# Kernel tuning notes

Hardware: AMD Instinct MI355X
Metric: run time of the kernel (lower is better)

The kernel has to match this reference:

```python
import jax, jax.numpy as jnp
import numpy as np

NUM_NODES = 10000  # fixed by input spec: edge_index values in [0, 10000)


def setup_inputs() -> dict:
    key = jax.random.key(0)
    k1, k2, k3 = jax.random.split(key, 3)
    N, E, D_IN, D_OUT = NUM_NODES, 320000, 256, 256
    x = jax.random.normal(k1, (N, D_IN), dtype=jnp.float32)
    edge_index = jax.random.randint(k2, (2, E), 0, N, dtype=jnp.int64)
    # ensure node N-1 appears so num_nodes == N as in the torch code
    edge_index = edge_index.at[0, 0].set(N - 1)
    # xavier_uniform for [D_IN, D_OUT]
    limit = float(np.sqrt(6.0 / (D_IN + D_OUT)))
    weight = jax.random.uniform(k3, (D_IN, D_OUT), dtype=jnp.float32,
                                minval=-limit, maxval=limit)
    return {"x": x, "edge_index": edge_index, "weight": weight}


def _normalize_adjacency(edge_index, num_nodes):
    src, dst = edge_index[0], edge_index[1]
    ones = jnp.ones(src.shape[0], dtype=jnp.float32)
    # symmetric binarized adjacency: adj[i,j] = adj[j,i] = 1 (set, not add)
    adj = jnp.zeros((num_nodes, num_nodes), dtype=jnp.float32)
    adj = adj.at[src, dst].max(ones)
    adj = adj.at[dst, src].max(ones)
    # one round of self-loops: adj += I
    adj = adj + jnp.eye(num_nodes, dtype=jnp.float32)
    deg = jnp.sum(adj, axis=1)                    # [N]
    dinv = 1.0 / jnp.sqrt(deg)                    # [N]
    # D^-1/2 A D^-1/2 via broadcasting (equivalent to diag mms)
    return adj * dinv[:, None] * dinv[None, :]


def reference(x, edge_index, weight):
    adj = _normalize_adjacency(edge_index, NUM_NODES)  # [N, N]
    h = adj @ x                                        # [N, D_IN]
    return h @ weight                                  # [N, D_OUT]
```

## Files before the change

kernel.cpp:

```cpp
#include <hip/hip_runtime.h>
#include <hip/hip_bf16.h>
#include <stdint.h>

#define N_NODES   10000
#define D_FEAT    256
#define E_EDGES   320000
#define ROW_WORDS 313
#define LIST_CAP  1024

#define NB     1000
#define RPB    10
#define B_CAP  1024
#define NBLK_E 313
#define NBLK_W 64
#define NBLK_C 1000
#define NBLK_G 625
#define COLSTR 128

#define LDSTR 264

typedef __attribute__((ext_vector_type(4))) float float4v;
typedef _Float16 half8  __attribute__((ext_vector_type(8)));
typedef _Float16 half4v __attribute__((ext_vector_type(4)));

__device__ __forceinline__ float h2f_lo(uint32_t u) {
    union { uint32_t u; _Float16 h[2]; } v; v.u = u; return (float)v.h[0];
}
__device__ __forceinline__ float h2f_hi(uint32_t u) {
    union { uint32_t u; _Float16 h[2]; } v; v.u = u; return (float)v.h[1];
}


__global__ void __launch_bounds__(1024)
scatter_wcast(const int* __restrict__ ei, uint32_t* __restrict__ bitmap,
              const float* __restrict__ w, _Float16* __restrict__ wt) {
    __shared__ float st[1024];
    int t = threadIdx.x;

    if (blockIdx.x >= NBLK_E) {
        int kb = (blockIdx.x - NBLK_E) * 4;
        int k = kb + (t >> 8), n = t & 255;
        st[(n << 2) | (t >> 8)] = w[(size_t)k * D_FEAT + n];
        __syncthreads();
        if (t < 256) {
            half4v o = { (_Float16)st[t * 4 + 0], (_Float16)st[t * 4 + 1],
                         (_Float16)st[t * 4 + 2], (_Float16)st[t * 4 + 3] };
            *(half4v*)&wt[(size_t)t * D_FEAT + kb] = o;
        }
        return;
    }

    int e = blockIdx.x * 1024 + t;
    if (e >= E_EDGES) return;
    int s = ei[e], d = ei[E_EDGES + e];
    if ((uint32_t)s >= N_NODES || (uint32_t)d >= N_NODES) return;
    atomicOr(&bitmap[(size_t)s * ROW_WORDS + (d >> 5)], 1u << (d & 31));
    atomicOr(&bitmap[(size_t)d * ROW_WORDS + (s >> 5)], 1u << (s & 31));
}

__global__ void __launch_bounds__(1024)
gemm_popc(const uint32_t* __restrict__ bitmap, float* __restrict__ dinv,
          const float* __restrict__ x, const _Float16* __restrict__ wt,
          _Float16* __restrict__ yw) {
    __shared__ __align__(16) _Float16 a_lds[16 * LDSTR];
    int t = threadIdx.x;

    if (blockIdx.x < NBLK_G) {
        int r0 = blockIdx.x * 16;
        int row = t >> 6, c4 = (t & 63) * 4;
        float4v xv = *(const float4v*)(x + (size_t)(r0 + row) * D_FEAT + c4);
        half4v h = { (_Float16)xv[0], (_Float16)xv[1],
                     (_Float16)xv[2], (_Float16)xv[3] };
        *(half4v*)&a_lds[row * LDSTR + c4] = h;
        __syncthreads();
        int wv = t >> 6, lane = t & 63;
        int quad = lane >> 4, r = lane & 15;
        int ct = wv;
        const _Float16* pb = wt + (size_t)(ct * 16 + r) * D_FEAT + quad * 8;
        float4v acc = {0.f, 0.f, 0.f, 0.f};
        #pragma unroll
        for (int kk = 0; kk < D_FEAT; kk += 32) {
            half8 a = *(const half8*)&a_lds[r * LDSTR + kk + quad * 8];
            half8 b = *(const half8*)(pb + kk);
            acc = __builtin_amdgcn_mfma_f32_16x16x32_f16(a, b, acc, 0, 0, 0);
        }
        int colg = ct * 16 + r;
        #pragma unroll
        for (int u = 0; u < 4; u++)
            yw[(size_t)(r0 + quad * 4 + u) * D_FEAT + colg] = (_Float16)acc[u];
        return;
    }

    int wv = t >> 6, lane = t & 63;
    int i = (blockIdx.x - NBLK_G) * 16 + wv;
    const uint32_t* rb = bitmap + (size_t)i * ROW_WORDS;
    int pop = 0;
    #pragma unroll
    for (int k = 0; k < 5; k++) {
        int w = lane + 64 * k;
        if (w < ROW_WORDS) pop += __popc(rb[w]);
    }
    #pragma unroll
    for (int off = 32; off > 0; off >>= 1) pop += __shfl_xor(pop, off, 64);
    if (lane == 0) dinv[i] = 1.0f / sqrtf((float)(pop + 1));
}

__global__ void __launch_bounds__(256)
spmm_bm(const uint32_t* __restrict__ bitmap, const float* __restrict__ dinv,
        const _Float16* __restrict__ ywp, float* __restrict__ out) {
    __shared__ __align__(16) uint32_t lists[4][LIST_CAP];
    const uint16_t* yw = (const uint16_t*)ywp;
    int wv = threadIdx.x >> 6, lane = threadIdx.x & 63;
    int i = blockIdx.x * 4 + wv;
    uint32_t* list = lists[wv];
    const uint32_t* rb = bitmap + (size_t)i * ROW_WORDS;

    uint32_t wbits[5]; int tot = 0;
    #pragma unroll
    for (int k = 0; k < 5; k++) {
        int w = lane + 64 * k;
        uint32_t b = (w < ROW_WORDS) ? rb[w] : 0u;
        wbits[k] = b;
        tot += __popc(b);
    }
    int incl = tot;
    #pragma unroll
    for (int off = 1; off < 64; off <<= 1) {
        int v = __shfl_up(incl, off, 64);
        if (lane >= off) incl += v;
    }
    uint32_t p = (uint32_t)(incl - tot);
    uint32_t deg = (uint32_t)__shfl(incl, 63, 64);
    #pragma unroll
    for (int k = 0; k < 5; k++) {
        uint32_t bits = wbits[k];
        uint32_t cbase = (uint32_t)(lane + 64 * k) << 5;
        while (bits) {
            if (p < LIST_CAP) list[p] = cbase + (uint32_t)__builtin_ctz(bits);
            p++;
            bits &= bits - 1;
        }
    }
    if (deg > LIST_CAP) deg = LIST_CAP;

    float di = dinv[i];
    size_t ch = (size_t)lane * 4;
    float4v z = {0.f, 0.f, 0.f, 0.f};
    float4v a0 = z, a1 = z, a2 = z, a3 = z, a4 = z, a5 = z, a6 = z, a7 = z;
    uint32_t t8 = deg & ~7u;
    uint32_t t = 0;
    for (; t < t8; t += 8) {
        uint4 jv0 = *(const uint4*)&list[t];
        uint4 jv1 = *(const uint4*)&list[t + 4];
        uint32_t j0 = jv0.x, j1 = jv0.y, j2 = jv0.z, j3 = jv0.w;
        uint32_t j4 = jv1.x, j5 = jv1.y, j6 = jv1.z, j7 = jv1.w;
        float d0 = dinv[j0], d1 = dinv[j1], d2 = dinv[j2], d3 = dinv[j3];
        float d4 = dinv[j4], d5 = dinv[j5], d6 = dinv[j6], d7 = dinv[j7];
        uint2 g0 = *(const uint2*)(yw + (size_t)j0 * D_FEAT + ch);
        uint2 g1 = *(const uint2*)(yw + (size_t)j1 * D_FEAT + ch);
        uint2 g2 = *(const uint2*)(yw + (size_t)j2 * D_FEAT + ch);
        uint2 g3 = *(const uint2*)(yw + (size_t)j3 * D_FEAT + ch);
        uint2 g4 = *(const uint2*)(yw + (size_t)j4 * D_FEAT + ch);
        uint2 g5 = *(const uint2*)(yw + (size_t)j5 * D_FEAT + ch);
        uint2 g6 = *(const uint2*)(yw + (size_t)j6 * D_FEAT + ch);
        uint2 g7 = *(const uint2*)(yw + (size_t)j7 * D_FEAT + ch);
        a0[0] += d0 * h2f_lo(g0.x); a0[1] += d0 * h2f_hi(g0.x);
        a0[2] += d0 * h2f_lo(g0.y); a0[3] += d0 * h2f_hi(g0.y);
        a1[0] += d1 * h2f_lo(g1.x); a1[1] += d1 * h2f_hi(g1.x);
        a1[2] += d1 * h2f_lo(g1.y); a1[3] += d1 * h2f_hi(g1.y);
        a2[0] += d2 * h2f_lo(g2.x); a2[1] += d2 * h2f_hi(g2.x);
        a2[2] += d2 * h2f_lo(g2.y); a2[3] += d2 * h2f_hi(g2.y);
        a3[0] += d3 * h2f_lo(g3.x); a3[1] += d3 * h2f_hi(g3.x);
        a3[2] += d3 * h2f_lo(g3.y); a3[3] += d3 * h2f_hi(g3.y);
        a4[0] += d4 * h2f_lo(g4.x); a4[1] += d4 * h2f_hi(g4.x);
        a4[2] += d4 * h2f_lo(g4.y); a4[3] += d4 * h2f_hi(g4.y);
        a5[0] += d5 * h2f_lo(g5.x); a5[1] += d5 * h2f_hi(g5.x);
        a5[2] += d5 * h2f_lo(g5.y); a5[3] += d5 * h2f_hi(g5.y);
        a6[0] += d6 * h2f_lo(g6.x); a6[1] += d6 * h2f_hi(g6.x);
        a6[2] += d6 * h2f_lo(g6.y); a6[3] += d6 * h2f_hi(g6.y);
        a7[0] += d7 * h2f_lo(g7.x); a7[1] += d7 * h2f_hi(g7.x);
        a7[2] += d7 * h2f_lo(g7.y); a7[3] += d7 * h2f_hi(g7.y);
    }
    for (; t < deg; t++) {
        uint32_t j = list[t];
        float dj = dinv[j];
        uint2 g = *(const uint2*)(yw + (size_t)j * D_FEAT + ch);
        a0[0] += dj * h2f_lo(g.x); a0[1] += dj * h2f_hi(g.x);
        a0[2] += dj * h2f_lo(g.y); a0[3] += dj * h2f_hi(g.y);
    }
    uint2 gs = *(const uint2*)(yw + (size_t)i * D_FEAT + ch);
    a1[0] += di * h2f_lo(gs.x); a1[1] += di * h2f_hi(gs.x);
    a1[2] += di * h2f_lo(gs.y); a1[3] += di * h2f_hi(gs.y);
    float4v acc = ((a0 + a1) + (a2 + a3)) + ((a4 + a5) + (a6 + a7));
    *(float4v*)(out + (size_t)i * D_FEAT + ch) = di * acc;
}


__global__ void __launch_bounds__(1024)
fill_sort(const int* __restrict__ ei, uint32_t* __restrict__ bucketbuf,
          uint32_t* __restrict__ cursors,
          const float* __restrict__ w, _Float16* __restrict__ wt) {
    __shared__ uint32_t hist[1024];
    __shared__ uint32_t lofs[1024];
    __shared__ uint32_t base_s[1024];
    __shared__ uint32_t wsum[16];
    __shared__ uint32_t stage[2048];
    __shared__ uint16_t sbkt[2048];
    int t = threadIdx.x;

    if (blockIdx.x >= NBLK_E) {
        int kb = (blockIdx.x - NBLK_E) * 4;
        int k = kb + (t >> 8), n = t & 255;
        float* st = (float*)stage;
        st[(n << 2) | (t >> 8)] = w[(size_t)k * D_FEAT + n];
        __syncthreads();
        if (t < 256) {
            half4v o = { (_Float16)st[t * 4 + 0], (_Float16)st[t * 4 + 1],
                         (_Float16)st[t * 4 + 2], (_Float16)st[t * 4 + 3] };
            *(half4v*)&wt[(size_t)t * D_FEAT + kb] = o;
        }
        return;
    }

    int wv = t >> 6, lane = t & 63;
    hist[t] = 0;
    __syncthreads();
    int e = blockIdx.x * 1024 + t;
    int b0 = -1, b1 = -1; uint32_t ent0 = 0, ent1 = 0, s0 = 0, s1 = 0;
    if (e < E_EDGES) {
        int s = ei[e], d = ei[E_EDGES + e];
        if ((uint32_t)s < N_NODES && (uint32_t)d < N_NODES) {
            b0 = s / RPB; ent0 = ((uint32_t)(s - b0 * RPB) << 14) | (uint32_t)d;
            b1 = d / RPB; ent1 = ((uint32_t)(d - b1 * RPB) << 14) | (uint32_t)s;
            s0 = atomicAdd(&hist[b0], 1u);
            s1 = atomicAdd(&hist[b1], 1u);
        }
    }
    __syncthreads();
    uint32_t h = hist[t];
    uint32_t incl = h;
    #pragma unroll
    for (int off = 1; off < 64; off <<= 1) {
        uint32_t v = __shfl_up(incl, off, 64);
        if (lane >= off) incl += v;
    }
    if (lane == 63) wsum[wv] = incl;
    __syncthreads();
    if (wv == 0) {
        uint32_t s = (lane < 16) ? wsum[lane] : 0u;
        #pragma unroll
        for (int off = 1; off < 16; off <<= 1) {
            uint32_t v = __shfl_up(s, off, 64);
            if (lane >= off) s += v;
        }
        if (lane < 16) wsum[lane] = s;
    }
    __syncthreads();
    uint32_t wbase = wv ? wsum[wv - 1] : 0u;
    lofs[t] = incl + wbase;
    base_s[t] = h ? atomicAdd(&cursors[t], h) : 0u;
    __syncthreads();
    if (b0 >= 0) {
        uint32_t p0 = lofs[b0] - hist[b0] + s0;
        stage[p0] = ent0; sbkt[p0] = (uint16_t)b0;
        uint32_t p1 = lofs[b1] - hist[b1] + s1;
        stage[p1] = ent1; sbkt[p1] = (uint16_t)b1;
    }
    __syncthreads();
    uint32_t total = lofs[1023];
    for (uint32_t idx = t; idx < total; idx += 1024) {
        uint32_t b = sbkt[idx];
        uint32_t pos = base_s[b] + (idx - (lofs[b] - hist[b]));
        if (pos < B_CAP) bucketbuf[(size_t)b * B_CAP + pos] = stage[idx];
    }
}

__global__ void __launch_bounds__(1024)
csr_gemm(const uint32_t* __restrict__ bucketbuf, const uint32_t* __restrict__ cursors,
         uint32_t* __restrict__ row_deg, float* __restrict__ dinv,
         uint16_t* __restrict__ col,
         const float* __restrict__ x, const _Float16* __restrict__ wt,
         _Float16* __restrict__ yw) {
    __shared__ __align__(16) uint32_t smem[RPB * ROW_WORDS];
    int t = threadIdx.x;

    if (blockIdx.x >= NBLK_C) {
        _Float16* a_lds = (_Float16*)smem;
        int r0 = (blockIdx.x - NBLK_C) * 16;
        int row = t >> 6, c4 = (t & 63) * 4;
        float4v xv = *(const float4v*)(x + (size_t)(r0 + row) * D_FEAT + c4);
        half4v h = { (_Float16)xv[0], (_Float16)xv[1],
                     (_Float16)xv[2], (_Float16)xv[3] };
        *(half4v*)&a_lds[row * LDSTR + c4] = h;
        __syncthreads();
        int wv = t >> 6, lane = t & 63;
        int quad = lane >> 4, r = lane & 15;
        int ct = wv;
        const _Float16* pb = wt + (size_t)(ct * 16 + r) * D_FEAT + quad * 8;
        float4v acc = {0.f, 0.f, 0.f, 0.f};
        #pragma unroll
        for (int kk = 0; kk < D_FEAT; kk += 32) {
            half8 a = *(const half8*)&a_lds[r * LDSTR + kk + quad * 8];
            half8 b = *(const half8*)(pb + kk);
            acc = __builtin_amdgcn_mfma_f32_16x16x32_f16(a, b, acc, 0, 0, 0);
        }
        int colg = ct * 16 + r;
        #pragma unroll
        for (int u = 0; u < 4; u++)
            yw[(size_t)(r0 + quad * 4 + u) * D_FEAT + colg] = (_Float16)acc[u];
        return;
    }

    uint32_t* bm = smem;
    int b = blockIdx.x;
    for (int i = t; i < RPB * ROW_WORDS; i += 1024) bm[i] = 0;
    __syncthreads();
    uint32_t cnt = min(cursors[b], (uint32_t)B_CAP);
    const uint32_t* bb = bucketbuf + (size_t)b * B_CAP;
    for (uint32_t i = t; i < cnt; i += 1024) {
        uint32_t ent = bb[i];
        uint32_t lr = ent >> 14, d = ent & 0x3FFFu;
        atomicOr(&bm[lr * ROW_WORDS + (d >> 5)], 1u << (d & 31));
    }
    __syncthreads();
    int wv = t >> 6, lane = t & 63;
    if (wv < RPB) {
        int r = wv;
        int gi = b * RPB + r;
        uint32_t wb[5]; int tot = 0;
        #pragma unroll
        for (int k = 0; k < 5; k++) {
            int w = lane + 64 * k;
            uint32_t v = (w < ROW_WORDS) ? bm[r * ROW_WORDS + w] : 0u;
            wb[k] = v; tot += __popc(v);
        }
        int incl = tot;
        #pragma unroll
        for (int off = 1; off < 64; off <<= 1) {
            int v = __shfl_up(incl, off, 64);
            if (lane >= off) incl += v;
        }
        uint32_t total = (uint32_t)__shfl(incl, 63, 64);
        if (lane == 0) {
            row_deg[gi] = min(total, (uint32_t)COLSTR);
            dinv[gi]    = 1.0f / sqrtf((float)(total + 1u));
        }
        uint32_t p = (uint32_t)(incl - tot);
        #pragma unroll
        for (int k = 0; k < 5; k++) {
            uint32_t bits = wb[k];
            uint32_t cbase = (uint32_t)(lane + 64 * k) << 5;
            while (bits) {
                if (p < COLSTR)
                    col[(size_t)gi * COLSTR + p] =
                        (uint16_t)(cbase + (uint32_t)__builtin_ctz(bits));
                p++;
                bits &= bits - 1;
            }
        }
    }
}

__global__ void __launch_bounds__(256)
spmm_out(const uint32_t* __restrict__ row_deg, const float* __restrict__ dinv,
         const uint16_t* __restrict__ col, const _Float16* __restrict__ ywp,
         float* __restrict__ out) {
    const uint16_t* yw = (const uint16_t*)ywp;
    int wv = threadIdx.x >> 6, lane = threadIdx.x & 63;
    int half = lane >> 5, sl = lane & 31;
    int i = blockIdx.x * 4 + wv;
    uint32_t base = (uint32_t)i * COLSTR;
    uint32_t deg = min(row_deg[i], (uint32_t)COLSTR);
    float di = dinv[i];
    size_t ch = (size_t)sl * 8;
    float4v z = {0.f, 0.f, 0.f, 0.f};
    float4v accl[8], acch[8];
    #pragma unroll
    for (int k = 0; k < 8; k++) { accl[k] = z; acch[k] = z; }

    uint32_t hb = (uint32_t)(half << 3);
    uint4 cv = {0u, 0u, 0u, 0u};
    if (deg) cv = *(const uint4*)&col[base + hb];

    for (uint32_t t = 0; t < deg; t += 16) {
        uint4 cvn = {0u, 0u, 0u, 0u};
        uint32_t tn = t + 16;
        if (tn < deg) cvn = *(const uint4*)&col[base + tn + hb];
        uint32_t tb = t + hb;
        uint32_t jr[8];
        jr[0] = cv.x & 0xffffu; jr[1] = cv.x >> 16;
        jr[2] = cv.y & 0xffffu; jr[3] = cv.y >> 16;
        jr[4] = cv.z & 0xffffu; jr[5] = cv.z >> 16;
        jr[6] = cv.w & 0xffffu; jr[7] = cv.w >> 16;
        uint4 g[8]; float dk[8];
        #pragma unroll
        for (int k = 0; k < 8; k++) {
            uint32_t j = min(jr[k], (uint32_t)(N_NODES - 1));
            g[k]  = *(const uint4*)(yw + ((size_t)j << 8) + ch);
            dk[k] = dinv[j];
        }
        #pragma unroll
        for (int k = 0; k < 8; k++) {
            float d = (tb + (uint32_t)k < deg) ? dk[k] : 0.f;
            accl[k][0] += d * h2f_lo(g[k].x); accl[k][1] += d * h2f_hi(g[k].x);
            accl[k][2] += d * h2f_lo(g[k].y); accl[k][3] += d * h2f_hi(g[k].y);
            acch[k][0] += d * h2f_lo(g[k].z); acch[k][1] += d * h2f_hi(g[k].z);
            acch[k][2] += d * h2f_lo(g[k].w); acch[k][3] += d * h2f_hi(g[k].w);
        }
        cv = cvn;
    }

    if (half == 0) {
        const uint4 gs = *(const uint4*)(yw + ((size_t)i << 8) + ch);
        accl[0][0] += di * h2f_lo(gs.x); accl[0][1] += di * h2f_hi(gs.x);
        accl[0][2] += di * h2f_lo(gs.y); accl[0][3] += di * h2f_hi(gs.y);
        acch[0][0] += di * h2f_lo(gs.z); acch[0][1] += di * h2f_hi(gs.z);
        acch[0][2] += di * h2f_lo(gs.w); acch[0][3] += di * h2f_hi(gs.w);
    }

    float4v lo = ((accl[0] + accl[1]) + (accl[2] + accl[3])) +
                 ((accl[4] + accl[5]) + (accl[6] + accl[7]));
    float4v hi = ((acch[0] + acch[1]) + (acch[2] + acch[3])) +
                 ((acch[4] + acch[5]) + (acch[6] + acch[7]));
    #pragma unroll
    for (int u = 0; u < 4; u++) {
        lo[u] += __shfl_xor(lo[u], 32, 64);
        hi[u] += __shfl_xor(hi[u], 32, 64);
    }
    float4v res;
    if (half) res = hi; else res = lo;
    float* op = out + (size_t)i * D_FEAT + (size_t)sl * 8 + (half ? 4 : 0);
    *(float4v*)op = di * res;
}

extern "C" void kernel_launch(void* const* d_in, const int* in_sizes, int n_in,
                              void* d_out, int out_size, void* d_ws, size_t ws_size,
                              hipStream_t stream) {
    const float* x  = (const float*)d_in[0];
    const int*   ei = (const int*)d_in[1];
    const float* w  = (const float*)d_in[2];
    float* out = (float*)d_out;
    uint8_t* ws = (uint8_t*)d_ws;

    const size_t T1_DI   = 12520000;
    const size_t T1_WT   = 12560000;
    const size_t T1_YW   = 12691072;
    const size_t NEED_T1 = 17811072;

    const size_t BB_OFF   = 4096;
    const size_t RD_OFF   = 4100096;
    const size_t DI_OFF   = 4140096;
    const size_t WT_OFF   = 4180096;
    const size_t YW_OFF   = 4311168;
    const size_t COL_OFF  = 9431168;
    const size_t NEED_T2  = 11991168;

    if (ws_size >= NEED_T1) {
        uint32_t* bitmap = (uint32_t*)ws;
        float*    dinv   = (float*)(ws + T1_DI);
        _Float16* wt     = (_Float16*)(ws + T1_WT);
        _Float16* yw     = (_Float16*)(ws + T1_YW);

        hipMemsetAsync(bitmap, 0, 12520000, stream);
        scatter_wcast<<<NBLK_E + NBLK_W, 1024, 0, stream>>>(ei, bitmap, w, wt);
        gemm_popc    <<<NBLK_G + 625, 1024, 0, stream>>>(bitmap, dinv, x, wt, yw);
        spmm_bm      <<<N_NODES / 4, 256, 0, stream>>>(bitmap, dinv, yw, out);
    } else if (ws_size >= NEED_T2) {
        uint32_t* cursors   = (uint32_t*)ws;
        uint32_t* bucketbuf = (uint32_t*)(ws + BB_OFF);
        uint32_t* row_deg   = (uint32_t*)(ws + RD_OFF);
        float*    dinv      = (float*)(ws + DI_OFF);
        _Float16* wt        = (_Float16*)(ws + WT_OFF);
        _Float16* yw        = (_Float16*)(ws + YW_OFF);
        uint16_t* col       = (uint16_t*)(ws + COL_OFF);

        hipMemsetAsync(cursors, 0, 4096, stream);
        fill_sort<<<NBLK_E + NBLK_W, 1024, 0, stream>>>(ei, bucketbuf, cursors, w, wt);
        csr_gemm <<<NBLK_C + NBLK_G, 1024, 0, stream>>>(bucketbuf, cursors,
                                                        row_deg, dinv, col, x, wt, yw);
        spmm_out <<<N_NODES / 4, 256, 0, stream>>>(row_deg, dinv, col, yw, out);
    }
}
```

Baseline: 140.4 us.

## Fuse scatter, GEMM and SpMM into one cooperative persistent kernel with grid syncs

Replaces the three launches (scatter+weight cast, gemm+degree, bitmap SpMM) with a single cooperative kernel of 1024 blocks of 256 threads, using grid.sync between phases and grid-stride loops. The aim is to remove per-launch overhead and inter-kernel gaps. In exchange, blocks shrink from 1024 to 256 threads, each GEMM block now covers four column tiles per wave, and grid-wide barriers add their own latency. If the cooperative launch fails, it falls back to the CSR path.

Result: slower. 405.4 us (+188.7%).

```diff
diff --git a/kernel.cpp b/kernel.cpp
--- a/kernel.cpp
+++ b/kernel.cpp
@@ -1,6 +1,9 @@
 #include <hip/hip_runtime.h>
+#include <hip/hip_cooperative_groups.h>
 #include <hip/hip_bf16.h>
 #include <stdint.h>
+
+namespace cg = cooperative_groups;
 
 #define N_NODES   10000
 #define D_FEAT    256
@@ -18,6 +21,7 @@
 #define COLSTR 128
 
 #define LDSTR 264
+#define GRID_C 1024
 
 typedef __attribute__((ext_vector_type(4))) float float4v;
 typedef _Float16 half8  __attribute__((ext_vector_type(8)));
@@ -30,169 +34,162 @@
     union { uint32_t u; _Float16 h[2]; } v; v.u = u; return (float)v.h[1];
 }
 
-
-__global__ void __launch_bounds__(1024)
-scatter_wcast(const int* __restrict__ ei, uint32_t* __restrict__ bitmap,
-              const float* __restrict__ w, _Float16* __restrict__ wt) {
-    __shared__ float st[1024];
+__global__ void __launch_bounds__(256, 4)
+fused_gcn(const int* __restrict__ ei, uint32_t* __restrict__ bitmap,
+          const float* __restrict__ w, _Float16* __restrict__ wt,
+          const float* __restrict__ x, float* __restrict__ dinv,
+          _Float16* __restrict__ yw, float* __restrict__ out) {
+    cg::grid_group grid = cg::this_grid();
+    __shared__ __align__(16) uint8_t smem[16384];
     int t = threadIdx.x;
-
-    if (blockIdx.x >= NBLK_E) {
-        int kb = (blockIdx.x - NBLK_E) * 4;
-        int k = kb + (t >> 8), n = t & 255;
-        st[(n << 2) | (t >> 8)] = w[(size_t)k * D_FEAT + n];
+    int bid = blockIdx.x;
+    int wv = t >> 6, lane = t & 63;
+
+    if (bid < 64) {
+        float* st = (float*)smem;
+        int kb = bid * 4;
+        for (int idx = t; idx < 1024; idx += 256)
+            st[idx] = w[(size_t)kb * D_FEAT + idx];
         __syncthreads();
-        if (t < 256) {
-            half4v o = { (_Float16)st[t * 4 + 0], (_Float16)st[t * 4 + 1],
-                         (_Float16)st[t * 4 + 2], (_Float16)st[t * 4 + 3] };
-            *(half4v*)&wt[(size_t)t * D_FEAT + kb] = o;
-        }
-        return;
-    }
-
-    int e = blockIdx.x * 1024 + t;
-    if (e >= E_EDGES) return;
-    int s = ei[e], d = ei[E_EDGES + e];
-    if ((uint32_t)s >= N_NODES || (uint32_t)d >= N_NODES) return;
-    atomicOr(&bitmap[(size_t)s * ROW_WORDS + (d >> 5)], 1u << (d & 31));
-    atomicOr(&bitmap[(size_t)d * ROW_WORDS + (s >> 5)], 1u << (s & 31));
-}
-
-__global__ void __launch_bounds__(1024)
-gemm_popc(const uint32_t* __restrict__ bitmap, float* __restrict__ dinv,
-          const float* __restrict__ x, const _Float16* __restrict__ wt,
-          _Float16* __restrict__ yw) {
-    __shared__ __align__(16) _Float16 a_lds[16 * LDSTR];
-    int t = threadIdx.x;
-
-    if (blockIdx.x < NBLK_G) {
-        int r0 = blockIdx.x * 16;
-        int row = t >> 6, c4 = (t & 63) * 4;
-        float4v xv = *(const float4v*)(x + (size_t)(r0 + row) * D_FEAT + c4);
-        half4v h = { (_Float16)xv[0], (_Float16)xv[1],
-                     (_Float16)xv[2], (_Float16)xv[3] };
-        *(half4v*)&a_lds[row * LDSTR + c4] = h;
+        int n = t;
+        half4v o = { (_Float16)st[0 * 256 + n], (_Float16)st[1 * 256 + n],
+                     (_Float16)st[2 * 256 + n], (_Float16)st[3 * 256 + n] };
+        *(half4v*)&wt[(size_t)n * D_FEAT + kb] = o;
+    }
+    for (int e = bid * 256 + t; e < E_EDGES; e += GRID_C * 256) {
+        int s = ei[e], d = ei[E_EDGES + e];
+        if ((uint32_t)s < N_NODES && (uint32_t)d < N_NODES) {
+            atomicOr(&bitmap[(size_t)s * ROW_WORDS + (d >> 5)], 1u << (d & 31));
+            atomicOr(&bitmap[(size_t)d * ROW_WORDS + (s >> 5)], 1u << (s & 31));
+        }
+    }
+    grid.sync();
+
+    if (bid < NBLK_G) {
+        _Float16* a_lds = (_Float16*)smem;
+        int r0 = bid * 16;
+        for (int idx = t; idx < 1024; idx += 256) {
+            int row = idx >> 6, c4 = (idx & 63) * 4;
+            float4v xv = *(const float4v*)(x + (size_t)(r0 + row) * D_FEAT + c4);
+            half4v h = { (_Float16)xv[0], (_Float16)xv[1],
+                         (_Float16)xv[2], (_Float16)xv[3] };
+            *(half4v*)&a_lds[row * LDSTR + c4] = h;
+        }
         __syncthreads();
-        int wv = t >> 6, lane = t & 63;
         int quad = lane >> 4, r = lane & 15;
-        int ct = wv;
-        const _Float16* pb = wt + (size_t)(ct * 16 + r) * D_FEAT + quad * 8;
-        float4v acc = {0.f, 0.f, 0.f, 0.f};
-        #pragma unroll
-        for (int kk = 0; kk < D_FEAT; kk += 32) {
-            half8 a = *(const half8*)&a_lds[r * LDSTR + kk + quad * 8];
-            half8 b = *(const half8*)(pb + kk);
-            acc = __builtin_amdgcn_mfma_f32_16x16x32_f16(a, b, acc, 0, 0, 0);
-        }
-        int colg = ct * 16 + r;
-        #pragma unroll
-        for (int u = 0; u < 4; u++)
-            yw[(size_t)(r0 + quad * 4 + u) * D_FEAT + colg] = (_Float16)acc[u];
-        return;
-    }
-
-    int wv = t >> 6, lane = t & 63;
-    int i = (blockIdx.x - NBLK_G) * 16 + wv;
-    const uint32_t* rb = bitmap + (size_t)i * ROW_WORDS;
-    int pop = 0;
-    #pragma unroll
-    for (int k = 0; k < 5; k++) {
-        int w = lane + 64 * k;
-        if (w < ROW_WORDS) pop += __popc(rb[w]);
-    }
-    #pragma unroll
-    for (int off = 32; off > 0; off >>= 1) pop += __shfl_xor(pop, off, 64);
-    if (lane == 0) dinv[i] = 1.0f / sqrtf((float)(pop + 1));
-}
-
-__global__ void __launch_bounds__(256)
-spmm_bm(const uint32_t* __restrict__ bitmap, const float* __restrict__ dinv,
-        const _Float16* __restrict__ ywp, float* __restrict__ out) {
-    __shared__ __align__(16) uint32_t lists[4][LIST_CAP];
-    const uint16_t* yw = (const uint16_t*)ywp;
-    int wv = threadIdx.x >> 6, lane = threadIdx.x & 63;
-    int i = blockIdx.x * 4 + wv;
-    uint32_t* list = lists[wv];
-    const uint32_t* rb = bitmap + (size_t)i * ROW_WORDS;
-
-    uint32_t wbits[5]; int tot = 0;
-    #pragma unroll
-    for (int k = 0; k < 5; k++) {
-        int w = lane + 64 * k;
-        uint32_t b = (w < ROW_WORDS) ? rb[w] : 0u;
-        wbits[k] = b;
-        tot += __popc(b);
-    }
-    int incl = tot;
-    #pragma unroll
-    for (int off = 1; off < 64; off <<= 1) {
-        int v = __shfl_up(incl, off, 64);
-        if (lane >= off) incl += v;
-    }
-    uint32_t p = (uint32_t)(incl - tot);
-    uint32_t deg = (uint32_t)__shfl(incl, 63, 64);
-    #pragma unroll
-    for (int k = 0; k < 5; k++) {
-        uint32_t bits = wbits[k];
-        uint32_t cbase = (uint32_t)(lane + 64 * k) << 5;
-        while (bits) {
-            if (p < LIST_CAP) list[p] = cbase + (uint32_t)__builtin_ctz(bits);
-            p++;
-            bits &= bits - 1;
-        }
-    }
-    if (deg > LIST_CAP) deg = LIST_CAP;
-
-    float di = dinv[i];
-    size_t ch = (size_t)lane * 4;
-    float4v z = {0.f, 0.f, 0.f, 0.f};
-    float4v a0 = z, a1 = z, a2 = z, a3 = z, a4 = z, a5 = z, a6 = z, a7 = z;
-    uint32_t t8 = deg & ~7u;
-    uint32_t t = 0;
-    for (; t < t8; t += 8) {
-        uint4 jv0 = *(const uint4*)&list[t];
-        uint4 jv1 = *(const uint4*)&list[t + 4];
-        uint32_t j0 = jv0.x, j1 = jv0.y, j2 = jv0.z, j3 = jv0.w;
-        uint32_t j4 = jv1.x, j5 = jv1.y, j6 = jv1.z, j7 = jv1.w;
-        float d0 = dinv[j0], d1 = dinv[j1], d2 = dinv[j2], d3 = dinv[j3];
-        float d4 = dinv[j4], d5 = dinv[j5], d6 = dinv[j6], d7 = dinv[j7];
-        uint2 g0 = *(const uint2*)(yw + (size_t)j0 * D_FEAT + ch);
-        uint2 g1 = *(const uint2*)(yw + (size_t)j1 * D_FEAT + ch);
-        uint2 g2 = *(const uint2*)(yw + (size_t)j2 * D_FEAT + ch);
-        uint2 g3 = *(const uint2*)(yw + (size_t)j3 * D_FEAT + ch);
-        uint2 g4 = *(const uint2*)(yw + (size_t)j4 * D_FEAT + ch);
-        uint2 g5 = *(const uint2*)(yw + (size_t)j5 * D_FEAT + ch);
-        uint2 g6 = *(const uint2*)(yw + (size_t)j6 * D_FEAT + ch);
-        uint2 g7 = *(const uint2*)(yw + (size_t)j7 * D_FEAT + ch);
-        a0[0] += d0 * h2f_lo(g0.x); a0[1] += d0 * h2f_hi(g0.x);
-        a0[2] += d0 * h2f_lo(g0.y); a0[3] += d0 * h2f_hi(g0.y);
-        a1[0] += d1 * h2f_lo(g1.x); a1[1] += d1 * h2f_hi(g1.x);
-        a1[2] += d1 * h2f_lo(g1.y); a1[3] += d1 * h2f_hi(g1.y);
-        a2[0] += d2 * h2f_lo(g2.x); a2[1] += d2 * h2f_hi(g2.x);
-        a2[2] += d2 * h2f_lo(g2.y); a2[3] += d2 * h2f_hi(g2.y);
-        a3[0] += d3 * h2f_lo(g3.x); a3[1] += d3 * h2f_hi(g3.x);
-        a3[2] += d3 * h2f_lo(g3.y); a3[3] += d3 * h2f_hi(g3.y);
-        a4[0] += d4 * h2f_lo(g4.x); a4[1] += d4 * h2f_hi(g4.x);
-        a4[2] += d4 * h2f_lo(g4.y); a4[3] += d4 * h2f_hi(g4.y);
-        a5[0] += d5 * h2f_lo(g5.x); a5[1] += d5 * h2f_hi(g5.x);
-        a5[2] += d5 * h2f_lo(g5.y); a5[3] += d5 * h2f_hi(g5.y);
-        a6[0] += d6 * h2f_lo(g6.x); a6[1] += d6 * h2f_hi(g6.x);
-        a6[2] += d6 * h2f_lo(g6.y); a6[3] += d6 * h2f_hi(g6.y);
-        a7[0] += d7 * h2f_lo(g7.x); a7[1] += d7 * h2f_hi(g7.x);
-        a7[2] += d7 * h2f_lo(g7.y); a7[3] += d7 * h2f_hi(g7.y);
-    }
-    for (; t < deg; t++) {
-        uint32_t j = list[t];
-        float dj = dinv[j];
-        uint2 g = *(const uint2*)(yw + (size_t)j * D_FEAT + ch);
-        a0[0] += dj * h2f_lo(g.x); a0[1] += dj * h2f_hi(g.x);
-        a0[2] += dj * h2f_lo(g.y); a0[3] += dj * h2f_hi(g.y);
-    }
-    uint2 gs = *(const uint2*)(yw + (size_t)i * D_FEAT + ch);
-    a1[0] += di * h2f_lo(gs.x); a1[1] += di * h2f_hi(gs.x);
-    a1[2] += di * h2f_lo(gs.y); a1[3] += di * h2f_hi(gs.y);
-    float4v acc = ((a0 + a1) + (a2 + a3)) + ((a4 + a5) + (a6 + a7));
-    *(float4v*)(out + (size_t)i * D_FEAT + ch) = di * acc;
+        for (int s = 0; s < 4; s++) {
+            int ct = wv * 4 + s;
+            const _Float16* pb = wt + (size_t)(ct * 16 + r) * D_FEAT + quad * 8;
+            float4v acc = {0.f, 0.f, 0.f, 0.f};
+            #pragma unroll
+            for (int kk = 0; kk < D_FEAT; kk += 32) {
+                half8 a = *(const half8*)&a_lds[r * LDSTR + kk + quad * 8];
+                half8 b = *(const half8*)(pb + kk);
+                acc = __builtin_amdgcn_mfma_f32_16x16x32_f16(a, b, acc, 0, 0, 0);
+            }
+            int colg = ct * 16 + r;
+            #pragma unroll
+            for (int u = 0; u < 4; u++)
+                yw[(size_t)(r0 + quad * 4 + u) * D_FEAT + colg] = (_Float16)acc[u];
+        }
+    }
+    for (int i = bid * 4 + wv; i < N_NODES; i += GRID_C * 4) {
+        const uint32_t* rb = bitmap + (size_t)i * ROW_WORDS;
+        int pop = 0;
+        #pragma unroll
+        for (int k = 0; k < 5; k++) {
+            int ww = lane + 64 * k;
+            if (ww < ROW_WORDS) pop += __popc(rb[ww]);
+        }
+        #pragma unroll
+        for (int off = 32; off > 0; off >>= 1) pop += __shfl_xor(pop, off, 64);
+        if (lane == 0) dinv[i] = 1.0f / sqrtf((float)(pop + 1));
+    }
+    grid.sync();
+
+    const uint16_t* ywu = (const uint16_t*)yw;
+    uint32_t* list = (uint32_t*)smem + (size_t)wv * LIST_CAP;
+    for (int i = bid * 4 + wv; i < N_NODES; i += GRID_C * 4) {
+        const uint32_t* rb = bitmap + (size_t)i * ROW_WORDS;
+        uint32_t wbits[5]; int tot = 0;
+        #pragma unroll
+        for (int k = 0; k < 5; k++) {
+            int ww = lane + 64 * k;
+            uint32_t b = (ww < ROW_WORDS) ? rb[ww] : 0u;
+            wbits[k] = b;
+            tot += __popc(b);
+        }
+        int incl = tot;
+        #pragma unroll
+        for (int off = 1; off < 64; off <<= 1) {
+            int v = __shfl_up(incl, off, 64);
+            if (lane >= off) incl += v;
+        }
+        uint32_t p = (uint32_t)(incl - tot);
+        uint32_t deg = (uint32_t)__shfl(incl, 63, 64);
+        #pragma unroll
+        for (int k = 0; k < 5; k++) {
+            uint32_t bits = wbits[k];
+            uint32_t cbase = (uint32_t)(lane + 64 * k) << 5;
+            while (bits) {
+                if (p < LIST_CAP) list[p] = cbase + (uint32_t)__builtin_ctz(bits);
+                p++;
+                bits &= bits - 1;
+            }
+        }
+        if (deg > LIST_CAP) deg = LIST_CAP;
+
+        float di = dinv[i];
+        size_t ch = (size_t)lane * 4;
+        float4v z = {0.f, 0.f, 0.f, 0.f};
+        float4v a0 = z, a1 = z, a2 = z, a3 = z, a4 = z, a5 = z, a6 = z, a7 = z;
+        uint32_t t8 = deg & ~7u;
+        uint32_t tt = 0;
+        for (; tt < t8; tt += 8) {
+            uint4 jv0 = *(const uint4*)&list[tt];
+            uint4 jv1 = *(const uint4*)&list[tt + 4];
+            uint32_t j0 = jv0.x, j1 = jv0.y, j2 = jv0.z, j3 = jv0.w;
+            uint32_t j4 = jv1.x, j5 = jv1.y, j6 = jv1.z, j7 = jv1.w;
+            float d0 = dinv[j0], d1 = dinv[j1], d2 = dinv[j2], d3 = dinv[j3];
+            float d4 = dinv[j4], d5 = dinv[j5], d6 = dinv[j6], d7 = dinv[j7];
+            uint2 g0 = *(const uint2*)(ywu + (size_t)j0 * D_FEAT + ch);
+            uint2 g1 = *(const uint2*)(ywu + (size_t)j1 * D_FEAT + ch);
+            uint2 g2 = *(const uint2*)(ywu + (size_t)j2 * D_FEAT + ch);
+            uint2 g3 = *(const uint2*)(ywu + (size_t)j3 * D_FEAT + ch);
+            uint2 g4 = *(const uint2*)(ywu + (size_t)j4 * D_FEAT + ch);
+            uint2 g5 = *(const uint2*)(ywu + (size_t)j5 * D_FEAT + ch);
+            uint2 g6 = *(const uint2*)(ywu + (size_t)j6 * D_FEAT + ch);
+            uint2 g7 = *(const uint2*)(ywu + (size_t)j7 * D_FEAT + ch);
+            a0[0] += d0 * h2f_lo(g0.x); a0[1] += d0 * h2f_hi(g0.x);
+            a0[2] += d0 * h2f_lo(g0.y); a0[3] += d0 * h2f_hi(g0.y);
+            a1[0] += d1 * h2f_lo(g1.x); a1[1] += d1 * h2f_hi(g1.x);
+            a1[2] += d1 * h2f_lo(g1.y); a1[3] += d1 * h2f_hi(g1.y);
+            a2[0] += d2 * h2f_lo(g2.x); a2[1] += d2 * h2f_hi(g2.x);
+            a2[2] += d2 * h2f_lo(g2.y); a2[3] += d2 * h2f_hi(g2.y);
+            a3[0] += d3 * h2f_lo(g3.x); a3[1] += d3 * h2f_hi(g3.x);
+            a3[2] += d3 * h2f_lo(g3.y); a3[3] += d3 * h2f_hi(g3.y);
+            a4[0] += d4 * h2f_lo(g4.x); a4[1] += d4 * h2f_hi(g4.x);
+            a4[2] += d4 * h2f_lo(g4.y); a4[3] += d4 * h2f_hi(g4.y);
+            a5[0] += d5 * h2f_lo(g5.x); a5[1] += d5 * h2f_hi(g5.x);
+            a5[2] += d5 * h2f_lo(g5.y); a5[3] += d5 * h2f_hi(g5.y);
+            a6[0] += d6 * h2f_lo(g6.x); a6[1] += d6 * h2f_hi(g6.x);
+            a6[2] += d6 * h2f_lo(g6.y); a6[3] += d6 * h2f_hi(g6.y);
+            a7[0] += d7 * h2f_lo(g7.x); a7[1] += d7 * h2f_hi(g7.x);
+            a7[2] += d7 * h2f_lo(g7.y); a7[3] += d7 * h2f_hi(g7.y);
+        }
+        for (; tt < deg; tt++) {
+            uint32_t j = list[tt];
+            float dj = dinv[j];
+            uint2 g = *(const uint2*)(ywu + (size_t)j * D_FEAT + ch);
+            a0[0] += dj * h2f_lo(g.x); a0[1] += dj * h2f_hi(g.x);
+            a0[2] += dj * h2f_lo(g.y); a0[3] += dj * h2f_hi(g.y);
+        }
+        uint2 gs = *(const uint2*)(ywu + (size_t)i * D_FEAT + ch);
+        a1[0] += di * h2f_lo(gs.x); a1[1] += di * h2f_hi(gs.x);
+        a1[2] += di * h2f_lo(gs.y); a1[3] += di * h2f_hi(gs.y);
+        float4v acc = ((a0 + a1) + (a2 + a3)) + ((a4 + a5) + (a6 + a7));
+        *(float4v*)(out + (size_t)i * D_FEAT + ch) = di * acc;
+    }
 }
 
 
@@ -462,10 +459,14 @@
         _Float16* yw     = (_Float16*)(ws + T1_YW);
 
         hipMemsetAsync(bitmap, 0, 12520000, stream);
-        scatter_wcast<<<NBLK_E + NBLK_W, 1024, 0, stream>>>(ei, bitmap, w, wt);
-        gemm_popc    <<<NBLK_G + 625, 1024, 0, stream>>>(bitmap, dinv, x, wt, yw);
-        spmm_bm      <<<N_NODES / 4, 256, 0, stream>>>(bitmap, dinv, yw, out);
-    } else if (ws_size >= NEED_T2) {
+        void* kargs[] = { (void*)&ei, (void*)&bitmap, (void*)&w, (void*)&wt,
+                          (void*)&x,  (void*)&dinv,   (void*)&yw, (void*)&out };
+        hipError_t err = hipLaunchCooperativeKernel(
+            (void*)fused_gcn, dim3(GRID_C), dim3(256), kargs, 0, stream);
+        if (err == hipSuccess) return;
+        (void)hipGetLastError();
+    }
+    if (ws_size >= NEED_T2) {
         uint32_t* cursors   = (uint32_t*)ws;
         uint32_t* bucketbuf = (uint32_t*)(ws + BB_OFF);
         uint32_t* row_deg   = (uint32_t*)(ws + RD_OFF);
```
